# Performance work log

Hardware: AMD Instinct MI355X
Metric: run time of the kernel (lower is better)

The kernel has to match this reference:

```python
import jax, jax.numpy as jnp
import numpy as np

BIG = 1e4  # larger than any image dimension; safe in fp32 when squared


def _edt(e):
    # e: [H, W] binary float mask. Exact Euclidean distance transform:
    # distance from each nonzero pixel to the nearest zero pixel
    # (matches cv2.distanceTransform(e, cv2.DIST_L2, maskSize=0)).
    H, W = e.shape
    zero = e == 0
    x = jnp.arange(W, dtype=jnp.float32)[None, :]            # [1, W]
    # 1D pass along rows: distance (in x) to nearest zero in the same row
    last = jax.lax.cummax(jnp.where(zero, x, -BIG), axis=1)              # nearest zero to the left
    nxt = -jax.lax.cummax(jnp.where(zero, -x, -BIG), axis=1, reverse=True)  # nearest zero to the right
    g = jnp.minimum(x - last, nxt - x)                        # [H, W], BIG-ish if row has no zero
    g2 = jnp.minimum(g, BIG) ** 2                             # squared row distance
    # 2D pass along columns: dist2[y, x] = min_r g2[r, x] + (y - r)^2 (exact EDT)
    y = jnp.arange(H, dtype=jnp.float32)
    d2 = (y[:, None] - y[None, :]) ** 2                       # [H, H]
    dist2 = jnp.min(g2[None, :, :] + d2[:, :, None], axis=1)  # [H, W]
    return jnp.sqrt(dist2)


def _min_max_norm(d):
    lo, hi = d.min(), d.max()
    return (d - lo) / (hi - lo + 1e-8)


def _edge_weight(edge):
    # edge: [B, 1, H, W] binary float
    e = edge[:, 0]  # [B, H, W]
    # lax.map keeps peak memory to one [H,H,W] candidate tensor at a time
    w = jax.lax.map(lambda ei: _min_max_norm(_edt(ei)), e)
    return w[:, None]  # [B, 1, H, W]


def setup_inputs() -> dict:
    key = jax.random.key(0)
    k1, k2, k3, k4 = jax.random.split(key, 4)
    shape = (16, 1, 384, 384)
    eps = 1e-4
    pred = jax.random.uniform(k1, shape, jnp.float32, eps, 1.0 - eps)
    pred_edge = jax.random.uniform(k2, shape, jnp.float32, eps, 1.0 - eps)
    label = jax.random.randint(k3, shape, 0, 2).astype(jnp.float32)
    edge = jax.random.randint(k4, shape, 0, 2).astype(jnp.float32)
    return {"pred": pred, "pred_edge": pred_edge, "label": label, "edge": edge}


def reference(pred, pred_edge, label, edge):
    Wm = _edge_weight(edge)  # [B, 1, H, W] in [0, 1]
    label_loss = jnp.mean(
        -(label * jnp.log(pred) + (1.0 - label) * jnp.log(1.0 - pred)) * (1.0 + Wm)
    )
    edge_loss = jnp.mean(
        -(edge * jnp.log(pred_edge) + (1.0 - edge) * jnp.log(1.0 - pred_edge))
    )
    return label_loss + edge_loss
```

## Files before the change

kernel.cpp:

```cpp
#include <hip/hip_runtime.h>

typedef unsigned long long u64;
typedef unsigned int u32;

#define NIMG 16
#define H 384
#define W 384
#define NPIX (H*W)
#define NTOT (NIMG*NPIX)
#define FBIG 10000.0f

#define RPB 96
#define NRB 4
#define NCT 12
#define EBLOCKS (NCT*NRB*NIMG)
#define NROW (NIMG*H)

__device__ __forceinline__ float bflo(u32 w){ return __uint_as_float(w<<16); }
__device__ __forceinline__ float bfhi(u32 w){ return __uint_as_float(w & 0xFFFF0000u); }

__device__ __forceinline__ void detect_flag(const u32* lw, int tid, u32* sflag) {
    if (tid < 64) {
        u32 a = 0;
        #pragma unroll
        for (int k = 0; k < 4; ++k) a |= lw[(tid & 63)*4 + k] & 0xFFFFu;
        u64 b = __ballot(a != 0u);
        if (tid == 0) *sflag = (b != 0ull) ? 1u : 0u;
    }
}

__global__ __launch_bounds__(256) void rowscan_kernel(
        const void* __restrict__ e, const u32* __restrict__ label_u32,
        float* __restrict__ g2) {
    __shared__ u32 sflag;
    int tid = threadIdx.x;
    detect_flag(label_u32, tid, &sflag);
    __syncthreads();
    bool isb = (sflag != 0u);

    int lane = tid & 63;
    int row  = blockIdx.x * 4 + (tid >> 6);

    u64 zm[6];
    if (isb) {
        const unsigned short* er = (const unsigned short*)e + (size_t)row * W;
        #pragma unroll
        for (int t = 0; t < 6; ++t) zm[t] = __ballot(er[t*64 + lane] == 0);
    } else {
        const float* er = (const float*)e + (size_t)row * W;
        #pragma unroll
        for (int t = 0; t < 6; ++t) zm[t] = __ballot(er[t*64 + lane] == 0.0f);
    }

    float* gr = g2 + (size_t)row * W;
    #pragma unroll
    for (int t = 0; t < 6; ++t) {
        int c = t*64 + lane;
        u64 m = zm[t] & ((lane == 63) ? ~0ull : ((1ull << (lane+1)) - 1ull));
        int tt = t;
        while (m == 0ull && tt > 0) m = zm[--tt];
        float dl = m ? (float)(c - (tt*64 + 63 - __builtin_clzll(m)))
                     : ((float)c + FBIG);
        m = zm[t] & ((lane == 0) ? ~0ull : ~((1ull << lane) - 1ull));
        tt = t;
        while (m == 0ull && tt < 5) m = zm[++tt];
        float dr = m ? (float)((tt*64 + __builtin_ctzll(m)) - c)
                     : (FBIG - (float)c);
        float g = fminf(fminf(dl, dr), FBIG);
        gr[c] = g * g;
    }
}

__global__ __launch_bounds__(256) void edt_loss_kernel(
    const float* __restrict__ g2,
    const void* __restrict__ pred, const void* __restrict__ pred_edge,
    const void* __restrict__ label, const void* __restrict__ edge,
    float* __restrict__ partials) {

    __shared__ float tileF[H * 32];
    __shared__ u32 sflag;
    __shared__ float cr[4][5];

    int tid  = threadIdx.x;
    int img  = blockIdx.z;
    int c0   = blockIdx.x * 32;
    int r0   = blockIdx.y * RPB;
    int lane = tid & 63;
    int wv   = tid >> 6;

    detect_flag((const u32*)label, tid, &sflag);

    const float* g2i = g2 + (size_t)img * NPIX;
    float4* tile4w = (float4*)tileF;
    #pragma unroll
    for (int k = 0; k < 12; ++k) {
        int gi  = tid + 256*k;
        int row = gi >> 3, c2 = gi & 7;
        tile4w[gi] = *(const float4*)(g2i + row * W + c0 + c2 * 4);
    }
    __syncthreads();
    bool isb = (sflag != 0u);

    const float4* tile4 = (const float4*)tileF;
    int c2t = tid & 7;
    int rg  = tid >> 3;
    int rb  = r0 + rg;

    uint4 st_p[3], st_q[3], st_l[3], st_e[3];
    #pragma unroll
    for (int i = 0; i < 3; ++i) {
        size_t base = (size_t)img * NPIX + (size_t)(rb + 32*i) * W + c0 + c2t * 4;
        if (isb) {
            uint2 a = *(const uint2*)((const unsigned short*)pred      + base);
            uint2 b = *(const uint2*)((const unsigned short*)pred_edge + base);
            uint2 c = *(const uint2*)((const unsigned short*)label     + base);
            uint2 d = *(const uint2*)((const unsigned short*)edge      + base);
            st_p[i].x=a.x; st_p[i].y=a.y; st_q[i].x=b.x; st_q[i].y=b.y;
            st_l[i].x=c.x; st_l[i].y=c.y; st_e[i].x=d.x; st_e[i].y=d.y;
        } else {
            st_p[i] = *(const uint4*)((const float*)pred      + base);
            st_q[i] = *(const uint4*)((const float*)pred_edge + base);
            st_l[i] = *(const uint4*)((const float*)label     + base);
            st_e[i] = *(const uint4*)((const float*)edge      + base);
        }
    }

    float4 best[3];
    float ub = 0.0f;
    #pragma unroll
    for (int i = 0; i < 3; ++i) {
        best[i] = tile4[(rb + 32*i)*8 + c2t];
        ub = fmaxf(ub, fmaxf(fmaxf(best[i].x, best[i].y), fmaxf(best[i].z, best[i].w)));
    }
    #pragma unroll
    for (int off = 1; off < 64; off <<= 1)
        ub = fmaxf(ub, __shfl_xor(ub, off));
    int jcap = (int)ceilf(sqrtf(ub)) + 1;
    if (jcap > H - 1) jcap = H - 1;

    for (int j = 1; j <= jcap; ++j) {
        float jj = (float)(j * j);
        #pragma unroll
        for (int i = 0; i < 3; ++i) {
            int r  = rb + 32*i;
            int ru = r - j; ru = (ru < 0) ? 0 : ru;
            int rd = r + j; rd = (rd > H-1) ? H-1 : rd;
            float4 vu = tile4[ru*8 + c2t];
            float4 vd = tile4[rd*8 + c2t];
            best[i].x = fminf(best[i].x, fminf(vu.x, vd.x) + jj);
            best[i].y = fminf(best[i].y, fminf(vu.y, vd.y) + jj);
            best[i].z = fminf(best[i].z, fminf(vu.z, vd.z) + jj);
            best[i].w = fminf(best[i].w, fminf(vu.w, vd.w) + jj);
        }
    }

    float sl = 0.0f, sd = 0.0f, se = 0.0f;
    float tmin = 3.0e38f, tmax = 0.0f;
    #pragma unroll
    for (int i = 0; i < 3; ++i) {
        float dv[4];
        dv[0] = sqrtf(best[i].x); dv[1] = sqrtf(best[i].y);
        dv[2] = sqrtf(best[i].z); dv[3] = sqrtf(best[i].w);
        #pragma unroll
        for (int cc = 0; cc < 4; ++cc) {
            tmin = fminf(tmin, dv[cc]);
            tmax = fmaxf(tmax, dv[cc]);
        }
        float p[4], q[4], lv[4], ev[4];
        if (isb) {
            p[0]=bflo(st_p[i].x); p[1]=bfhi(st_p[i].x); p[2]=bflo(st_p[i].y); p[3]=bfhi(st_p[i].y);
            q[0]=bflo(st_q[i].x); q[1]=bfhi(st_q[i].x); q[2]=bflo(st_q[i].y); q[3]=bfhi(st_q[i].y);
            lv[0]=bflo(st_l[i].x); lv[1]=bfhi(st_l[i].x); lv[2]=bflo(st_l[i].y); lv[3]=bfhi(st_l[i].y);
            ev[0]=bflo(st_e[i].x); ev[1]=bfhi(st_e[i].x); ev[2]=bflo(st_e[i].y); ev[3]=bfhi(st_e[i].y);
        } else {
            p[0]=__uint_as_float(st_p[i].x); p[1]=__uint_as_float(st_p[i].y);
            p[2]=__uint_as_float(st_p[i].z); p[3]=__uint_as_float(st_p[i].w);
            q[0]=__uint_as_float(st_q[i].x); q[1]=__uint_as_float(st_q[i].y);
            q[2]=__uint_as_float(st_q[i].z); q[3]=__uint_as_float(st_q[i].w);
            lv[0]=__uint_as_float(st_l[i].x); lv[1]=__uint_as_float(st_l[i].y);
            lv[2]=__uint_as_float(st_l[i].z); lv[3]=__uint_as_float(st_l[i].w);
            ev[0]=__uint_as_float(st_e[i].x); ev[1]=__uint_as_float(st_e[i].y);
            ev[2]=__uint_as_float(st_e[i].z); ev[3]=__uint_as_float(st_e[i].w);
        }
        #pragma unroll
        for (int cc = 0; cc < 4; ++cc) {
            float bl = -__logf((lv[cc] != 0.0f) ? p[cc] : 1.0f - p[cc]);
            sl += bl;
            sd = fmaf(bl, dv[cc], sd);
            se += -__logf((ev[cc] != 0.0f) ? q[cc] : 1.0f - q[cc]);
        }
    }

    #pragma unroll
    for (int off = 1; off < 64; off <<= 1) {
        sl += __shfl_xor(sl, off);
        sd += __shfl_xor(sd, off);
        se += __shfl_xor(se, off);
        tmin = fminf(tmin, __shfl_xor(tmin, off));
        tmax = fmaxf(tmax, __shfl_xor(tmax, off));
    }
    if (lane == 0) {
        cr[wv][0] = sl; cr[wv][1] = sd; cr[wv][2] = se;
        cr[wv][3] = tmin; cr[wv][4] = tmax;
    }
    __syncthreads();
    if (tid == 0) {
        float S1 = cr[0][0] + cr[1][0] + cr[2][0] + cr[3][0];
        float S2 = cr[0][1] + cr[1][1] + cr[2][1] + cr[3][1];
        float Se = cr[0][2] + cr[1][2] + cr[2][2] + cr[3][2];
        float Tm = fminf(fminf(cr[0][3], cr[1][3]), fminf(cr[2][3], cr[3][3]));
        float TM = fmaxf(fmaxf(cr[0][4], cr[1][4]), fmaxf(cr[2][4], cr[3][4]));
        int blk = (img * NRB + blockIdx.y) * NCT + blockIdx.x;
        float* pp = partials + blk * 5;
        pp[0] = S1; pp[1] = S2; pp[2] = Se; pp[3] = Tm; pp[4] = TM;
    }
}

__global__ void final_kernel(const float* __restrict__ partials,
                             u32* __restrict__ out) {
    __shared__ float a1[256], a2[256], a3[256], a4[256], a5[256];
    __shared__ float ci[NIMG], sei[NIMG];
    int tid = threadIdx.x;
    int img = tid >> 4, s = tid & 15;
    float S1 = 0.0f, S2 = 0.0f, Se = 0.0f, Tm = 3.0e38f, TM = 0.0f;
    #pragma unroll
    for (int k = 0; k < 3; ++k) {
        const float* pp = partials + (img * 48 + s + 16*k) * 5;
        S1 += pp[0]; S2 += pp[1]; Se += pp[2];
        Tm = fminf(Tm, pp[3]); TM = fmaxf(TM, pp[4]);
    }
    a1[tid]=S1; a2[tid]=S2; a3[tid]=Se; a4[tid]=Tm; a5[tid]=TM;
    __syncthreads();
    for (int st = 8; st > 0; st >>= 1) {
        if ((tid & 15) < st) {
            a1[tid] += a1[tid+st]; a2[tid] += a2[tid+st]; a3[tid] += a3[tid+st];
            a4[tid] = fminf(a4[tid], a4[tid+st]);
            a5[tid] = fmaxf(a5[tid], a5[tid+st]);
        }
        __syncthreads();
    }
    if ((tid & 15) == 0) {
        float lo = a4[tid], hi = a5[tid];
        float inv = 1.0f / (hi - lo + 1e-8f);
        ci[img]  = a1[tid] + (a2[tid] - lo * a1[tid]) * inv;
        sei[img] = a3[tid];
    }
    __syncthreads();
    if (tid == 0) {
        float t = 0.0f;
        for (int i = 0; i < NIMG; ++i) t += ci[i] + sei[i];
        float v = t / (float)NTOT;
        u32 fv = __float_as_uint(v);
        u32 b  = (fv + 0x7FFFu + ((fv >> 16) & 1u)) >> 16;
        out[0] = (fv & 0xFFFF0000u) | (b & 0xFFFFu);
    }
}

extern "C" void kernel_launch(void* const* d_in, const int* in_sizes, int n_in,
                              void* d_out, int out_size, void* d_ws, size_t ws_size,
                              hipStream_t stream) {
    float* ws = (float*)d_ws;
    float* g2 = ws;
    float* partials = ws + NTOT;

    rowscan_kernel<<<NROW / 4, 256, 0, stream>>>(d_in[3], (const u32*)d_in[2], g2);
    edt_loss_kernel<<<dim3(NCT, NRB, NIMG), 256, 0, stream>>>(
        g2, d_in[0], d_in[1], d_in[2], d_in[3], partials);
    final_kernel<<<1, 256, 0, stream>>>(partials, (u32*)d_out);
}
```

Measured before the change: 28.25 us.

## Store row distances as u16 and stage only a guarded row window in LDS

The row-scan pass now writes the unsquared integer row distance as 16-bit values instead of squared fp32, which halves intermediate traffic. The column pass loads only its 96 rows plus a 48-row guard band into shared memory, squaring on load, instead of staging the full 384-row column strip. Offsets beyond the guard fall back to direct global u16 reads. The smaller tile cuts global reads and LDS footprint, which may raise occupancy. Distant lookups become uncoalesced global loads when jcap exceeds the guard, and squaring the capped 10000 stays exact in fp32.

```diff
diff --git a/kernel.cpp b/kernel.cpp
--- a/kernel.cpp
+++ b/kernel.cpp
@@ -2,6 +2,7 @@
 
 typedef unsigned long long u64;
 typedef unsigned int u32;
+typedef unsigned short u16;
 
 #define NIMG 16
 #define H 384
@@ -9,12 +10,15 @@
 #define NPIX (H*W)
 #define NTOT (NIMG*NPIX)
 #define FBIG 10000.0f
+#define IBIG 10000
 
 #define RPB 96
 #define NRB 4
 #define NCT 12
 #define EBLOCKS (NCT*NRB*NIMG)
 #define NROW (NIMG*H)
+#define GUARD 48
+#define TROWS (RPB + 2*GUARD)
 
 __device__ __forceinline__ float bflo(u32 w){ return __uint_as_float(w<<16); }
 __device__ __forceinline__ float bfhi(u32 w){ return __uint_as_float(w & 0xFFFF0000u); }
@@ -31,7 +35,7 @@
 
 __global__ __launch_bounds__(256) void rowscan_kernel(
         const void* __restrict__ e, const u32* __restrict__ label_u32,
-        float* __restrict__ g2) {
+        u16* __restrict__ gq) {
     __shared__ u32 sflag;
     int tid = threadIdx.x;
     detect_flag(label_u32, tid, &sflag);
@@ -43,7 +47,7 @@
 
     u64 zm[6];
     if (isb) {
-        const unsigned short* er = (const unsigned short*)e + (size_t)row * W;
+        const u16* er = (const u16*)e + (size_t)row * W;
         #pragma unroll
         for (int t = 0; t < 6; ++t) zm[t] = __ballot(er[t*64 + lane] == 0);
     } else {
@@ -52,32 +56,30 @@
         for (int t = 0; t < 6; ++t) zm[t] = __ballot(er[t*64 + lane] == 0.0f);
     }
 
-    float* gr = g2 + (size_t)row * W;
+    u16* gr = gq + (size_t)row * W;
     #pragma unroll
     for (int t = 0; t < 6; ++t) {
         int c = t*64 + lane;
         u64 m = zm[t] & ((lane == 63) ? ~0ull : ((1ull << (lane+1)) - 1ull));
         int tt = t;
         while (m == 0ull && tt > 0) m = zm[--tt];
-        float dl = m ? (float)(c - (tt*64 + 63 - __builtin_clzll(m)))
-                     : ((float)c + FBIG);
+        int dl = m ? (c - (tt*64 + 63 - __builtin_clzll(m))) : 16777216;
         m = zm[t] & ((lane == 0) ? ~0ull : ~((1ull << lane) - 1ull));
         tt = t;
         while (m == 0ull && tt < 5) m = zm[++tt];
-        float dr = m ? (float)((tt*64 + __builtin_ctzll(m)) - c)
-                     : (FBIG - (float)c);
-        float g = fminf(fminf(dl, dr), FBIG);
-        gr[c] = g * g;
+        int dr = m ? ((tt*64 + __builtin_ctzll(m)) - c) : 16777216;
+        int g = min(min(dl, dr), IBIG);
+        gr[c] = (u16)g;
     }
 }
 
 __global__ __launch_bounds__(256) void edt_loss_kernel(
-    const float* __restrict__ g2,
+    const u16* __restrict__ gq,
     const void* __restrict__ pred, const void* __restrict__ pred_edge,
     const void* __restrict__ label, const void* __restrict__ edge,
     float* __restrict__ partials) {
 
-    __shared__ float tileF[H * 32];
+    __shared__ float tileF[TROWS * 32];
     __shared__ u32 sflag;
     __shared__ float cr[4][5];
 
@@ -90,13 +92,23 @@
 
     detect_flag((const u32*)label, tid, &sflag);
 
-    const float* g2i = g2 + (size_t)img * NPIX;
+    int ws = r0 - GUARD; ws = (ws < 0) ? 0 : ws;
+    int we = r0 + RPB + GUARD; we = (we > H) ? H : we;
+    int nrows = we - ws;
+
+    const u16* gi = gq + (size_t)img * NPIX;
     float4* tile4w = (float4*)tileF;
-    #pragma unroll
-    for (int k = 0; k < 12; ++k) {
-        int gi  = tid + 256*k;
-        int row = gi >> 3, c2 = gi & 7;
-        tile4w[gi] = *(const float4*)(g2i + row * W + c0 + c2 * 4);
+    int chunks = nrows * 8;
+    for (int k = 0; k < 6; ++k) {
+        int idx = tid + 256*k;
+        if (idx < chunks) {
+            int rl = idx >> 3, ch = idx & 7;
+            const u16* src = gi + (size_t)(ws + rl) * W + c0 + ch*4;
+            u32 w0 = *(const u32*)src, w1 = *(const u32*)(src + 2);
+            float a = (float)(w0 & 0xFFFFu), b = (float)(w0 >> 16);
+            float c = (float)(w1 & 0xFFFFu), d = (float)(w1 >> 16);
+            tile4w[idx] = make_float4(a*a, b*b, c*c, d*d);
+        }
     }
     __syncthreads();
     bool isb = (sflag != 0u);
@@ -111,10 +123,10 @@
     for (int i = 0; i < 3; ++i) {
         size_t base = (size_t)img * NPIX + (size_t)(rb + 32*i) * W + c0 + c2t * 4;
         if (isb) {
-            uint2 a = *(const uint2*)((const unsigned short*)pred      + base);
-            uint2 b = *(const uint2*)((const unsigned short*)pred_edge + base);
-            uint2 c = *(const uint2*)((const unsigned short*)label     + base);
-            uint2 d = *(const uint2*)((const unsigned short*)edge      + base);
+            uint2 a = *(const uint2*)((const u16*)pred      + base);
+            uint2 b = *(const uint2*)((const u16*)pred_edge + base);
+            uint2 c = *(const uint2*)((const u16*)label     + base);
+            uint2 d = *(const uint2*)((const u16*)edge      + base);
             st_p[i].x=a.x; st_p[i].y=a.y; st_q[i].x=b.x; st_q[i].y=b.y;
             st_l[i].x=c.x; st_l[i].y=c.y; st_e[i].x=d.x; st_e[i].y=d.y;
         } else {
@@ -129,7 +141,7 @@
     float ub = 0.0f;
     #pragma unroll
     for (int i = 0; i < 3; ++i) {
-        best[i] = tile4[(rb + 32*i)*8 + c2t];
+        best[i] = tile4[(rb + 32*i - ws)*8 + c2t];
         ub = fmaxf(ub, fmaxf(fmaxf(best[i].x, best[i].y), fmaxf(best[i].z, best[i].w)));
     }
     #pragma unroll
@@ -137,20 +149,42 @@
         ub = fmaxf(ub, __shfl_xor(ub, off));
     int jcap = (int)ceilf(sqrtf(ub)) + 1;
     if (jcap > H - 1) jcap = H - 1;
-
-    for (int j = 1; j <= jcap; ++j) {
+    int jfast = (jcap < GUARD) ? jcap : GUARD;
+
+    for (int j = 1; j <= jfast; ++j) {
         float jj = (float)(j * j);
         #pragma unroll
         for (int i = 0; i < 3; ++i) {
             int r  = rb + 32*i;
             int ru = r - j; ru = (ru < 0) ? 0 : ru;
             int rd = r + j; rd = (rd > H-1) ? H-1 : rd;
-            float4 vu = tile4[ru*8 + c2t];
-            float4 vd = tile4[rd*8 + c2t];
+            float4 vu = tile4[(ru - ws)*8 + c2t];
+            float4 vd = tile4[(rd - ws)*8 + c2t];
             best[i].x = fminf(best[i].x, fminf(vu.x, vd.x) + jj);
             best[i].y = fminf(best[i].y, fminf(vu.y, vd.y) + jj);
             best[i].z = fminf(best[i].z, fminf(vu.z, vd.z) + jj);
             best[i].w = fminf(best[i].w, fminf(vu.w, vd.w) + jj);
+        }
+    }
+    for (int j = GUARD + 1; j <= jcap; ++j) {
+        float jj = (float)(j * j);
+        #pragma unroll
+        for (int i = 0; i < 3; ++i) {
+            int r  = rb + 32*i;
+            int ru = r - j; ru = (ru < 0) ? 0 : ru;
+            int rd = r + j; rd = (rd > H-1) ? H-1 : rd;
+            const u16* su = gi + (size_t)ru * W + c0 + c2t*4;
+            const u16* sd = gi + (size_t)rd * W + c0 + c2t*4;
+            u32 u0 = *(const u32*)su, u1 = *(const u32*)(su+2);
+            u32 d0 = *(const u32*)sd, d1 = *(const u32*)(sd+2);
+            float ux = (float)(u0 & 0xFFFFu), uy = (float)(u0 >> 16);
+            float uz = (float)(u1 & 0xFFFFu), uw = (float)(u1 >> 16);
+            float dx = (float)(d0 & 0xFFFFu), dy = (float)(d0 >> 16);
+            float dz = (float)(d1 & 0xFFFFu), dw = (float)(d1 >> 16);
+            best[i].x = fminf(best[i].x, fminf(ux*ux, dx*dx) + jj);
+            best[i].y = fminf(best[i].y, fminf(uy*uy, dy*dy) + jj);
+            best[i].z = fminf(best[i].z, fminf(uz*uz, dz*dz) + jj);
+            best[i].w = fminf(best[i].w, fminf(uw*uw, dw*dw) + jj);
         }
     }
 
@@ -259,12 +293,11 @@
 extern "C" void kernel_launch(void* const* d_in, const int* in_sizes, int n_in,
                               void* d_out, int out_size, void* d_ws, size_t ws_size,
                               hipStream_t stream) {
-    float* ws = (float*)d_ws;
-    float* g2 = ws;
-    float* partials = ws + NTOT;
-
-    rowscan_kernel<<<NROW / 4, 256, 0, stream>>>(d_in[3], (const u32*)d_in[2], g2);
+    u16* gq = (u16*)d_ws;
+    float* partials = (float*)((char*)d_ws + (size_t)NTOT * sizeof(u16));
+
+    rowscan_kernel<<<NROW / 4, 256, 0, stream>>>(d_in[3], (const u32*)d_in[2], gq);
     edt_loss_kernel<<<dim3(NCT, NRB, NIMG), 256, 0, stream>>>(
-        g2, d_in[0], d_in[1], d_in[2], d_in[3], partials);
+        gq, d_in[0], d_in[1], d_in[2], d_in[3], partials);
     final_kernel<<<1, 256, 0, stream>>>(partials, (u32*)d_out);
 }
```

Result: no change. 28.16 us (-0.3%).
